# Optimization experiments

Measured on AMD Instinct MI355X. Metric: run time of the kernel, lower is better.

The kernel has to match this reference:

```python
import jax, jax.numpy as jnp
import numpy as np

NUM_EMBED = 1024
HEAD_SIZE = 64
B, T = 4, 4096

def setup_inputs() -> dict:
    key = jax.random.key(0)
    kx, kq, kk, kv = jax.random.split(key, 4)
    scale = NUM_EMBED ** -0.5
    return {
        "x": jax.random.normal(kx, (B, T, NUM_EMBED), dtype=jnp.float32),
        "Wq": jax.random.normal(kq, (NUM_EMBED, HEAD_SIZE), dtype=jnp.float32) * scale,
        "Wk": jax.random.normal(kk, (NUM_EMBED, HEAD_SIZE), dtype=jnp.float32) * scale,
        "Wv": jax.random.normal(kv, (NUM_EMBED, HEAD_SIZE), dtype=jnp.float32) * scale,
    }

def reference(x, Wq, Wk, Wv):
    # x: [B,T,C]; Wq/Wk/Wv: [C,H]
    q = jnp.einsum('btc,ch->bth', x, Wq)
    k = jnp.einsum('btc,ch->bth', x, Wk)
    v = jnp.einsum('btc,ch->bth', x, Wv)
    Tq = x.shape[1]
    att = jnp.einsum('bth,bsh->bts', q, k) * (k.shape[-1] ** -0.5)  # [B,T,T]
    causal = jnp.tril(jnp.ones((Tq, Tq), dtype=bool))
    att = jnp.where(causal, att, -jnp.inf)
    att = jax.nn.softmax(att, axis=-1)
    # dropout p=0 (eval mode): identity
    out = jnp.einsum('bts,bsh->bth', att, v)  # [B,T,H]
    return out
```

## Files before the change

### kernel.cpp

```cpp
#include <hip/hip_runtime.h>

#define B_ 4
#define T_ 4096
#define C_ 1024
#define H_ 64

typedef _Float16 half8  __attribute__((ext_vector_type(8)));
typedef _Float16 half4_ __attribute__((ext_vector_type(4)));
typedef float    floatx4 __attribute__((ext_vector_type(4)));

#define MFMA16(a, b, c) __builtin_amdgcn_mfma_f32_16x16x32_f16(a, b, c, 0, 0, 0)

__global__ __launch_bounds__(256) void pack_w_kn(
    const float* __restrict__ Wq, const float* __restrict__ Wk,
    const float* __restrict__ Wv, _Float16* __restrict__ Wt2)
{
    const int idx  = blockIdx.x * 256 + threadIdx.x;
    const int mt   = idx >> 14;
    const int j    = (idx >> 10) & 15;
    const int f    = (idx >> 9) & 1;
    const int lane = (idx >> 3) & 63;
    const int jj   = idx & 7;
    const int q = lane >> 4, c = lane & 15;
    const int k  = j * 64 + f * 32 + q * 8 + jj;
    const int hp = mt * 16 + c;
    const float* W = (hp < 64) ? Wq : (hp < 128) ? Wk : Wv;
    Wt2[idx] = (_Float16)W[k * H_ + (hp & 63)];
}

__global__ __launch_bounds__(512) void qkv_kn(
    const float* __restrict__ x, const _Float16* __restrict__ Wt2,
    _Float16* __restrict__ Qh, _Float16* __restrict__ Kpk,
    _Float16* __restrict__ Vpk)
{
    __shared__ _Float16 xs[2][32][72];
    const int tid  = threadIdx.x;
    const int lane = tid & 63, w = tid >> 6;
    const int q    = lane >> 4, c = lane & 15;
    const int nt   = w & 1;
    const int mg   = w >> 1;
    const int row0 = blockIdx.x * 32;

    const int srow = tid >> 4, scol = (tid & 15) * 4;
    const float* xg = x + (size_t)(row0 + srow) * C_ + scol;

    floatx4 acc[3];
    #pragma unroll
    for (int i = 0; i < 3; ++i) acc[i] = floatx4{0.f, 0.f, 0.f, 0.f};

    float4 g = *(const float4*)xg;

    for (int j = 0; j < 16; ++j) {
        half4_ hv;
        hv[0] = (_Float16)g.x; hv[1] = (_Float16)g.y;
        hv[2] = (_Float16)g.z; hv[3] = (_Float16)g.w;
        *(half4_*)(&xs[j & 1][srow][scol]) = hv;
        __syncthreads();
        if (j < 15) g = *(const float4*)(xg + (j + 1) * 64);

        const _Float16* xrow = &xs[j & 1][nt * 16 + c][q * 8];
        const half8 b0 = *(const half8*)xrow;
        const half8 b1 = *(const half8*)(xrow + 32);

        half8 a[6];
        #pragma unroll
        for (int i = 0; i < 3; ++i) {
            const size_t fb = ((size_t)((mg * 3 + i) * 16 + j) * 2) * 512 + lane * 8;
            a[i * 2]     = *(const half8*)(Wt2 + fb);
            a[i * 2 + 1] = *(const half8*)(Wt2 + fb + 512);
        }
        #pragma unroll
        for (int i = 0; i < 3; ++i) {
            acc[i] = MFMA16(a[i * 2],     b0, acc[i]);
            acc[i] = MFMA16(a[i * 2 + 1], b1, acc[i]);
        }
    }

    const int row = row0 + nt * 16 + c;
    const int b = row >> 12, t4 = row & (T_ - 1);
    const int kt = t4 >> 6;
    const size_t tbase = ((size_t)b * 64 + kt) * 4096;
    const int mtk = (t4 >> 4) & 3;
    const int kk  = t4 & 63;

    #pragma unroll
    for (int i = 0; i < 3; ++i) {
        const int gi = mg * 3 + i;
        if (gi < 4) {
            half4_ v;
            #pragma unroll
            for (int r = 0; r < 4; ++r) v[r] = (_Float16)acc[i][r];
            *(half4_*)(Qh + (size_t)row * H_ + gi * 16 + q * 4) = v;
        } else if (gi < 8) {
            half4_ v;
            #pragma unroll
            for (int r = 0; r < 4; ++r) v[r] = (_Float16)acc[i][r];
            const int e  = gi - 4;
            const int f  = e >> 1;
            const int qa = (e * 2 + (q >> 1)) & 3;
            *(half4_*)(Kpk + tbase + ((size_t)(mtk * 2 + f) * 64 + qa * 16 + c) * 8
                       + (q & 1) * 4) = v;
        } else {
            const int mtv = gi - 8;
            const int qa = (kk >> 3) & 3, fv = kk >> 5, jv = kk & 7;
            #pragma unroll
            for (int r = 0; r < 4; ++r) {
                const int cv = q * 4 + r;
                Vpk[tbase + ((size_t)(mtv * 2 + fv) * 64 + qa * 16 + cv) * 8 + jv]
                    = (_Float16)acc[i][r];
            }
        }
    }
}

__global__ __launch_bounds__(512, 4) void attn_kn(
    const _Float16* __restrict__ Qh, const _Float16* __restrict__ Kpk,
    const _Float16* __restrict__ Vpk, float* __restrict__ out)
{
    __shared__ __align__(16) char smem[36864];
    const int lane = threadIdx.x & 63;
    const int w    = threadIdx.x >> 6;
    const int q    = lane >> 4, c = lane & 15;
    const int b    = blockIdx.y;
    const int t    = 255 - (int)blockIdx.x;
    const int row0 = t * 16;
    const int grow = b * T_ + row0;
    const int nk   = (t >> 2) + 1;

    _Float16* Pw = (_Float16*)smem + w * 2304;

    half8 bq0 = *(const half8*)(Qh + (size_t)(grow + c) * H_ + q * 8);
    half8 bq1 = *(const half8*)(Qh + (size_t)(grow + c) * H_ + 32 + q * 8);
    const _Float16 qs = (_Float16)0.18033688f;
    bq0 *= qs; bq1 *= qs;

    floatx4 o[4];
    #pragma unroll
    for (int i = 0; i < 4; ++i) o[i] = floatx4{0.f, 0.f, 0.f, 0.f};
    float m = -3.0e38f, l = 0.f;

    for (int kt = w; kt < nk; kt += 8) {
        const int kb = kt * 64;
        const _Float16* Kt = Kpk + ((size_t)b * 64 + kt) * 4096;
        const _Float16* Vt = Vpk + ((size_t)b * 64 + kt) * 4096;
        half8 a0[4], a1[4];

        #pragma unroll
        for (int mt = 0; mt < 4; ++mt) {
            a0[mt] = *(const half8*)(Kt + ((size_t)(mt * 2)     * 64 + lane) * 8);
            a1[mt] = *(const half8*)(Kt + ((size_t)(mt * 2 + 1) * 64 + lane) * 8);
        }
        floatx4 s[4];
        #pragma unroll
        for (int mt = 0; mt < 4; ++mt) {
            floatx4 z = floatx4{0.f, 0.f, 0.f, 0.f};
            z = MFMA16(a0[mt], bq0, z);
            s[mt] = MFMA16(a1[mt], bq1, z);
        }
        #pragma unroll
        for (int mt = 0; mt < 4; ++mt) {
            a0[mt] = *(const half8*)(Vt + ((size_t)(mt * 2)     * 64 + lane) * 8);
            a1[mt] = *(const half8*)(Vt + ((size_t)(mt * 2 + 1) * 64 + lane) * 8);
        }

        if (kt == nk - 1) {
            #pragma unroll
            for (int mt = 0; mt < 4; ++mt)
                #pragma unroll
                for (int r = 0; r < 4; ++r)
                    if (kb + mt * 16 + q * 4 + r > row0 + c) s[mt][r] = -3.0e38f;
        }

        float mx = s[0][0];
        #pragma unroll
        for (int mt = 0; mt < 4; ++mt)
            #pragma unroll
            for (int r = 0; r < 4; ++r) mx = fmaxf(mx, s[mt][r]);
        mx = fmaxf(mx, __shfl_xor(mx, 16, 64));
        mx = fmaxf(mx, __shfl_xor(mx, 32, 64));
        const float mn    = fmaxf(m, mx);
        const float alpha = exp2f(m - mn);
        float p[4][4];
        float sl = 0.f;
        #pragma unroll
        for (int mt = 0; mt < 4; ++mt)
            #pragma unroll
            for (int r = 0; r < 4; ++r) {
                p[mt][r] = exp2f(s[mt][r] - mn);
                sl += p[mt][r];
            }
        sl += __shfl_xor(sl, 16, 64);
        sl += __shfl_xor(sl, 32, 64);
        l = l * alpha + sl;
        m = mn;
        #pragma unroll
        for (int mt = 0; mt < 4; ++mt)
            #pragma unroll
            for (int r = 0; r < 4; ++r) o[mt][r] *= alpha;

        _Float16* pl = Pw + ((kt >> 3) & 1) * 1152 + c * 72;
        #pragma unroll
        for (int mt = 0; mt < 4; ++mt) {
            half4_ ph;
            #pragma unroll
            for (int r = 0; r < 4; ++r) ph[r] = (_Float16)p[mt][r];
            *(half4_*)(pl + mt * 16 + q * 4) = ph;
        }
        const half8 bp0 = *(const half8*)(pl + q * 8);
        const half8 bp1 = *(const half8*)(pl + 32 + q * 8);

        #pragma unroll
        for (int mt = 0; mt < 4; ++mt) {
            o[mt] = MFMA16(a0[mt], bp0, o[mt]);
            o[mt] = MFMA16(a1[mt], bp1, o[mt]);
        }
    }

    __syncthreads();
    float* Ol = (float*)smem;
    float* Ml = (float*)(smem + 34816);
    float* Ll = (float*)(smem + 35328);
    if (q == 0) Ml[w * 16 + c] = m;
    __syncthreads();
    float M = Ml[c];
    #pragma unroll
    for (int w2 = 1; w2 < 8; ++w2) M = fmaxf(M, Ml[w2 * 16 + c]);
    const float alpha = exp2f(m - M);
    if (q == 0) Ll[w * 16 + c] = l * alpha;
    #pragma unroll
    for (int mt = 0; mt < 4; ++mt)
        #pragma unroll
        for (int r = 0; r < 4; ++r)
            Ol[w * 1088 + (mt * 16 + q * 4 + r) * 17 + c] = o[mt][r] * alpha;
    __syncthreads();

    float L = 0.f;
    #pragma unroll
    for (int w2 = 0; w2 < 8; ++w2) L += Ll[w2 * 16 + c];
    const float inv = 1.f / L;
    const int h0 = w * 8 + q * 2;
    float ox = 0.f, oy = 0.f;
    #pragma unroll
    for (int w2 = 0; w2 < 8; ++w2) {
        ox += Ol[w2 * 1088 + h0 * 17 + c];
        oy += Ol[w2 * 1088 + (h0 + 1) * 17 + c];
    }
    float2 st; st.x = ox * inv; st.y = oy * inv;
    *(float2*)(out + (size_t)(grow + c) * H_ + h0) = st;
}

extern "C" void kernel_launch(void* const* d_in, const int* in_sizes, int n_in,
                              void* d_out, int out_size, void* d_ws, size_t ws_size,
                              hipStream_t stream) {
    const float* x  = (const float*)d_in[0];
    const float* Wq = (const float*)d_in[1];
    const float* Wk = (const float*)d_in[2];
    const float* Wv = (const float*)d_in[3];
    float* out = (float*)d_out;

    _Float16* ws = (_Float16*)d_ws;
    _Float16* Wt2 = ws;
    _Float16* Qh  = ws + 196608;
    _Float16* Kpk = Qh + 1048576;
    _Float16* Vpk = Kpk + 1048576;

    hipLaunchKernelGGL(pack_w_kn, dim3(768), dim3(256), 0, stream, Wq, Wk, Wv, Wt2);
    hipLaunchKernelGGL(qkv_kn, dim3((B_ * T_) / 32), dim3(512), 0, stream,
                       x, Wt2, Qh, Kpk, Vpk);
    hipLaunchKernelGGL(attn_kn, dim3(T_ / 16, B_), dim3(512), 0, stream,
                       Qh, Kpk, Vpk, out);
}
```

Before: 142.7 us.

## Process two query/row tiles per wave to reuse K/V and weight fragments

The attention kernel now handles 32 query rows per block, two 16-row tiles per wave. Each K/V fragment loaded from global memory feeds twice as many MFMAs, which halves K/V traffic and the number of blocks. The QKV projection kernel likewise uses 4 waves that each cover both 16-row halves, so each weight fragment is reused twice. The cost is more registers: attention launch bounds drop to 3 blocks per SM, and the finishing reduction runs twice with extra barriers.

```diff
diff --git a/kernel.cpp b/kernel.cpp
--- a/kernel.cpp
+++ b/kernel.cpp
@@ -28,7 +28,7 @@
     Wt2[idx] = (_Float16)W[k * H_ + (hp & 63)];
 }
 
-__global__ __launch_bounds__(512) void qkv_kn(
+__global__ __launch_bounds__(256, 4) void qkv_kn(
     const float* __restrict__ x, const _Float16* __restrict__ Wt2,
     _Float16* __restrict__ Qh, _Float16* __restrict__ Kpk,
     _Float16* __restrict__ Vpk)
@@ -37,83 +37,93 @@
     const int tid  = threadIdx.x;
     const int lane = tid & 63, w = tid >> 6;
     const int q    = lane >> 4, c = lane & 15;
-    const int nt   = w & 1;
-    const int mg   = w >> 1;
     const int row0 = blockIdx.x * 32;
 
-    const int srow = tid >> 4, scol = (tid & 15) * 4;
-    const float* xg = x + (size_t)(row0 + srow) * C_ + scol;
-
-    floatx4 acc[3];
+    const int r1 = tid >> 4, c1 = (tid & 15) * 4;
+    const float* xg1 = x + (size_t)(row0 + r1) * C_ + c1;
+    const float* xg2 = xg1 + 16 * C_;
+
+    floatx4 acc[3][2];
     #pragma unroll
-    for (int i = 0; i < 3; ++i) acc[i] = floatx4{0.f, 0.f, 0.f, 0.f};
-
-    float4 g = *(const float4*)xg;
+    for (int i = 0; i < 3; ++i)
+        #pragma unroll
+        for (int n = 0; n < 2; ++n) acc[i][n] = floatx4{0.f, 0.f, 0.f, 0.f};
+
+    float4 g1 = *(const float4*)xg1;
+    float4 g2 = *(const float4*)xg2;
 
     for (int j = 0; j < 16; ++j) {
-        half4_ hv;
-        hv[0] = (_Float16)g.x; hv[1] = (_Float16)g.y;
-        hv[2] = (_Float16)g.z; hv[3] = (_Float16)g.w;
-        *(half4_*)(&xs[j & 1][srow][scol]) = hv;
+        half4_ h1, h2;
+        h1[0] = (_Float16)g1.x; h1[1] = (_Float16)g1.y;
+        h1[2] = (_Float16)g1.z; h1[3] = (_Float16)g1.w;
+        h2[0] = (_Float16)g2.x; h2[1] = (_Float16)g2.y;
+        h2[2] = (_Float16)g2.z; h2[3] = (_Float16)g2.w;
+        *(half4_*)(&xs[j & 1][r1][c1])      = h1;
+        *(half4_*)(&xs[j & 1][r1 + 16][c1]) = h2;
         __syncthreads();
-        if (j < 15) g = *(const float4*)(xg + (j + 1) * 64);
-
-        const _Float16* xrow = &xs[j & 1][nt * 16 + c][q * 8];
-        const half8 b0 = *(const half8*)xrow;
-        const half8 b1 = *(const half8*)(xrow + 32);
-
-        half8 a[6];
+        if (j < 15) {
+            g1 = *(const float4*)(xg1 + (j + 1) * 64);
+            g2 = *(const float4*)(xg2 + (j + 1) * 64);
+        }
+
+        const half8 b0 = *(const half8*)(&xs[j & 1][c][q * 8]);
+        const half8 b1 = *(const half8*)(&xs[j & 1][c][32 + q * 8]);
+        const half8 b2 = *(const half8*)(&xs[j & 1][16 + c][q * 8]);
+        const half8 b3 = *(const half8*)(&xs[j & 1][16 + c][32 + q * 8]);
+
         #pragma unroll
         for (int i = 0; i < 3; ++i) {
-            const size_t fb = ((size_t)((mg * 3 + i) * 16 + j) * 2) * 512 + lane * 8;
-            a[i * 2]     = *(const half8*)(Wt2 + fb);
-            a[i * 2 + 1] = *(const half8*)(Wt2 + fb + 512);
-        }
+            const size_t fb = ((size_t)((w * 3 + i) * 16 + j) * 2) * 512 + lane * 8;
+            const half8 a0 = *(const half8*)(Wt2 + fb);
+            const half8 a1 = *(const half8*)(Wt2 + fb + 512);
+            acc[i][0] = MFMA16(a0, b0, acc[i][0]);
+            acc[i][0] = MFMA16(a1, b1, acc[i][0]);
+            acc[i][1] = MFMA16(a0, b2, acc[i][1]);
+            acc[i][1] = MFMA16(a1, b3, acc[i][1]);
+        }
+    }
+
+    #pragma unroll
+    for (int n = 0; n < 2; ++n) {
+        const int row = row0 + n * 16 + c;
+        const int b = row >> 12, t4 = row & (T_ - 1);
+        const int kt = t4 >> 6;
+        const size_t tbase = ((size_t)b * 64 + kt) * 4096;
+        const int mtk = (t4 >> 4) & 3;
+        const int kk  = t4 & 63;
         #pragma unroll
         for (int i = 0; i < 3; ++i) {
-            acc[i] = MFMA16(a[i * 2],     b0, acc[i]);
-            acc[i] = MFMA16(a[i * 2 + 1], b1, acc[i]);
-        }
-    }
-
-    const int row = row0 + nt * 16 + c;
-    const int b = row >> 12, t4 = row & (T_ - 1);
-    const int kt = t4 >> 6;
-    const size_t tbase = ((size_t)b * 64 + kt) * 4096;
-    const int mtk = (t4 >> 4) & 3;
-    const int kk  = t4 & 63;
-
-    #pragma unroll
-    for (int i = 0; i < 3; ++i) {
-        const int gi = mg * 3 + i;
-        if (gi < 4) {
-            half4_ v;
-            #pragma unroll
-            for (int r = 0; r < 4; ++r) v[r] = (_Float16)acc[i][r];
-            *(half4_*)(Qh + (size_t)row * H_ + gi * 16 + q * 4) = v;
-        } else if (gi < 8) {
-            half4_ v;
-            #pragma unroll
-            for (int r = 0; r < 4; ++r) v[r] = (_Float16)acc[i][r];
-            const int e  = gi - 4;
-            const int f  = e >> 1;
-            const int qa = (e * 2 + (q >> 1)) & 3;
-            *(half4_*)(Kpk + tbase + ((size_t)(mtk * 2 + f) * 64 + qa * 16 + c) * 8
-                       + (q & 1) * 4) = v;
-        } else {
-            const int mtv = gi - 8;
-            const int qa = (kk >> 3) & 3, fv = kk >> 5, jv = kk & 7;
-            #pragma unroll
-            for (int r = 0; r < 4; ++r) {
-                const int cv = q * 4 + r;
-                Vpk[tbase + ((size_t)(mtv * 2 + fv) * 64 + qa * 16 + cv) * 8 + jv]
-                    = (_Float16)acc[i][r];
+            const int gi = w * 3 + i;
+            if (gi < 4) {
+                half4_ v;
+                #pragma unroll
+                for (int r = 0; r < 4; ++r) v[r] = (_Float16)acc[i][n][r];
+                *(half4_*)(Qh + (size_t)row * H_ + gi * 16 + q * 4) = v;
+            } else if (gi < 8) {
+                half4_ v;
+                #pragma unroll
+                for (int r = 0; r < 4; ++r) v[r] = (_Float16)acc[i][n][r];
+                const int e  = gi - 4;
+                const int f  = e >> 1;
+                const int qa = (e * 2 + (q >> 1)) & 3;
+                *(half4_*)(Kpk + tbase
+                           + ((size_t)(mtk * 2 + f) * 64 + qa * 16 + c) * 8
+                           + (q & 1) * 4) = v;
+            } else {
+                const int mtv = gi - 8;
+                const int qa = (kk >> 3) & 3, fv = kk >> 5, jv = kk & 7;
+                #pragma unroll
+                for (int r = 0; r < 4; ++r) {
+                    const int cv = q * 4 + r;
+                    Vpk[tbase + ((size_t)(mtv * 2 + fv) * 64 + qa * 16 + cv) * 8
+                        + jv] = (_Float16)acc[i][n][r];
+                }
             }
         }
     }
 }
 
-__global__ __launch_bounds__(512, 4) void attn_kn(
+__global__ __launch_bounds__(512, 3) void attn_kn(
     const _Float16* __restrict__ Qh, const _Float16* __restrict__ Kpk,
     const _Float16* __restrict__ Vpk, float* __restrict__ out)
 {
@@ -122,131 +132,184 @@
     const int w    = threadIdx.x >> 6;
     const int q    = lane >> 4, c = lane & 15;
     const int b    = blockIdx.y;
-    const int t    = 255 - (int)blockIdx.x;
-    const int row0 = t * 16;
+    const int t32  = 127 - (int)blockIdx.x;
+    const int row0 = t32 * 32;
     const int grow = b * T_ + row0;
-    const int nk   = (t >> 2) + 1;
-
-    _Float16* Pw = (_Float16*)smem + w * 2304;
-
+    const int nk   = (t32 >> 1) + 1;
+
+    _Float16* pl0 = (_Float16*)smem + w * 2304 + c * 72;
+    _Float16* pl1 = pl0 + 1152;
+
+    const _Float16 qs = (_Float16)0.18033688f;
     half8 bq0 = *(const half8*)(Qh + (size_t)(grow + c) * H_ + q * 8);
     half8 bq1 = *(const half8*)(Qh + (size_t)(grow + c) * H_ + 32 + q * 8);
-    const _Float16 qs = (_Float16)0.18033688f;
-    bq0 *= qs; bq1 *= qs;
-
-    floatx4 o[4];
+    half8 bq2 = *(const half8*)(Qh + (size_t)(grow + 16 + c) * H_ + q * 8);
+    half8 bq3 = *(const half8*)(Qh + (size_t)(grow + 16 + c) * H_ + 32 + q * 8);
+    bq0 *= qs; bq1 *= qs; bq2 *= qs; bq3 *= qs;
+
+    floatx4 o0[4], o1[4];
     #pragma unroll
-    for (int i = 0; i < 4; ++i) o[i] = floatx4{0.f, 0.f, 0.f, 0.f};
-    float m = -3.0e38f, l = 0.f;
+    for (int i = 0; i < 4; ++i) {
+        o0[i] = floatx4{0.f, 0.f, 0.f, 0.f};
+        o1[i] = floatx4{0.f, 0.f, 0.f, 0.f};
+    }
+    float m0 = -3.0e38f, l0 = 0.f, m1 = -3.0e38f, l1 = 0.f;
 
     for (int kt = w; kt < nk; kt += 8) {
         const int kb = kt * 64;
         const _Float16* Kt = Kpk + ((size_t)b * 64 + kt) * 4096;
         const _Float16* Vt = Vpk + ((size_t)b * 64 + kt) * 4096;
-        half8 a0[4], a1[4];
-
-        #pragma unroll
-        for (int mt = 0; mt < 4; ++mt) {
-            a0[mt] = *(const half8*)(Kt + ((size_t)(mt * 2)     * 64 + lane) * 8);
-            a1[mt] = *(const half8*)(Kt + ((size_t)(mt * 2 + 1) * 64 + lane) * 8);
-        }
-        floatx4 s[4];
+
+        half8 ka[4], kb8[4];
+        #pragma unroll
+        for (int mt = 0; mt < 4; ++mt) {
+            ka[mt]  = *(const half8*)(Kt + ((size_t)(mt * 2)     * 64 + lane) * 8);
+            kb8[mt] = *(const half8*)(Kt + ((size_t)(mt * 2 + 1) * 64 + lane) * 8);
+        }
+        floatx4 s0[4], s1[4];
         #pragma unroll
         for (int mt = 0; mt < 4; ++mt) {
             floatx4 z = floatx4{0.f, 0.f, 0.f, 0.f};
-            z = MFMA16(a0[mt], bq0, z);
-            s[mt] = MFMA16(a1[mt], bq1, z);
-        }
-        #pragma unroll
-        for (int mt = 0; mt < 4; ++mt) {
-            a0[mt] = *(const half8*)(Vt + ((size_t)(mt * 2)     * 64 + lane) * 8);
-            a1[mt] = *(const half8*)(Vt + ((size_t)(mt * 2 + 1) * 64 + lane) * 8);
+            z = MFMA16(ka[mt], bq0, z);
+            s0[mt] = MFMA16(kb8[mt], bq1, z);
+        }
+        half8 va[4], vb[4];
+        #pragma unroll
+        for (int mt = 0; mt < 4; ++mt) {
+            va[mt] = *(const half8*)(Vt + ((size_t)(mt * 2)     * 64 + lane) * 8);
+            vb[mt] = *(const half8*)(Vt + ((size_t)(mt * 2 + 1) * 64 + lane) * 8);
+        }
+        #pragma unroll
+        for (int mt = 0; mt < 4; ++mt) {
+            floatx4 z = floatx4{0.f, 0.f, 0.f, 0.f};
+            z = MFMA16(ka[mt], bq2, z);
+            s1[mt] = MFMA16(kb8[mt], bq3, z);
         }
 
         if (kt == nk - 1) {
             #pragma unroll
             for (int mt = 0; mt < 4; ++mt)
                 #pragma unroll
-                for (int r = 0; r < 4; ++r)
-                    if (kb + mt * 16 + q * 4 + r > row0 + c) s[mt][r] = -3.0e38f;
-        }
-
-        float mx = s[0][0];
-        #pragma unroll
-        for (int mt = 0; mt < 4; ++mt)
-            #pragma unroll
-            for (int r = 0; r < 4; ++r) mx = fmaxf(mx, s[mt][r]);
-        mx = fmaxf(mx, __shfl_xor(mx, 16, 64));
-        mx = fmaxf(mx, __shfl_xor(mx, 32, 64));
-        const float mn    = fmaxf(m, mx);
-        const float alpha = exp2f(m - mn);
-        float p[4][4];
-        float sl = 0.f;
-        #pragma unroll
-        for (int mt = 0; mt < 4; ++mt)
-            #pragma unroll
-            for (int r = 0; r < 4; ++r) {
-                p[mt][r] = exp2f(s[mt][r] - mn);
-                sl += p[mt][r];
+                for (int r = 0; r < 4; ++r) {
+                    const int key = kb + mt * 16 + q * 4 + r;
+                    if (key > row0 + c)      s0[mt][r] = -3.0e38f;
+                    if (key > row0 + 16 + c) s1[mt][r] = -3.0e38f;
+                }
+        }
+
+        {
+            float mx = s0[0][0];
+            #pragma unroll
+            for (int mt = 0; mt < 4; ++mt)
+                #pragma unroll
+                for (int r = 0; r < 4; ++r) mx = fmaxf(mx, s0[mt][r]);
+            mx = fmaxf(mx, __shfl_xor(mx, 16, 64));
+            mx = fmaxf(mx, __shfl_xor(mx, 32, 64));
+            const float mn    = fmaxf(m0, mx);
+            const float alpha = exp2f(m0 - mn);
+            float sl = 0.f;
+            #pragma unroll
+            for (int mt = 0; mt < 4; ++mt) {
+                half4_ ph;
+                #pragma unroll
+                for (int r = 0; r < 4; ++r) {
+                    const float p = exp2f(s0[mt][r] - mn);
+                    sl += p;
+                    ph[r] = (_Float16)p;
+                }
+                *(half4_*)(pl0 + mt * 16 + q * 4) = ph;
             }
-        sl += __shfl_xor(sl, 16, 64);
-        sl += __shfl_xor(sl, 32, 64);
-        l = l * alpha + sl;
-        m = mn;
-        #pragma unroll
-        for (int mt = 0; mt < 4; ++mt)
-            #pragma unroll
-            for (int r = 0; r < 4; ++r) o[mt][r] *= alpha;
-
-        _Float16* pl = Pw + ((kt >> 3) & 1) * 1152 + c * 72;
-        #pragma unroll
-        for (int mt = 0; mt < 4; ++mt) {
-            half4_ ph;
-            #pragma unroll
-            for (int r = 0; r < 4; ++r) ph[r] = (_Float16)p[mt][r];
-            *(half4_*)(pl + mt * 16 + q * 4) = ph;
-        }
-        const half8 bp0 = *(const half8*)(pl + q * 8);
-        const half8 bp1 = *(const half8*)(pl + 32 + q * 8);
-
-        #pragma unroll
-        for (int mt = 0; mt < 4; ++mt) {
-            o[mt] = MFMA16(a0[mt], bp0, o[mt]);
-            o[mt] = MFMA16(a1[mt], bp1, o[mt]);
-        }
-    }
-
-    __syncthreads();
+            sl += __shfl_xor(sl, 16, 64);
+            sl += __shfl_xor(sl, 32, 64);
+            l0 = l0 * alpha + sl;
+            m0 = mn;
+            #pragma unroll
+            for (int mt = 0; mt < 4; ++mt)
+                #pragma unroll
+                for (int r = 0; r < 4; ++r) o0[mt][r] *= alpha;
+        }
+        {
+            float mx = s1[0][0];
+            #pragma unroll
+            for (int mt = 0; mt < 4; ++mt)
+                #pragma unroll
+                for (int r = 0; r < 4; ++r) mx = fmaxf(mx, s1[mt][r]);
+            mx = fmaxf(mx, __shfl_xor(mx, 16, 64));
+            mx = fmaxf(mx, __shfl_xor(mx, 32, 64));
+            const float mn    = fmaxf(m1, mx);
+            const float alpha = exp2f(m1 - mn);
+            float sl = 0.f;
+            #pragma unroll
+            for (int mt = 0; mt < 4; ++mt) {
+                half4_ ph;
+                #pragma unroll
+                for (int r = 0; r < 4; ++r) {
+                    const float p = exp2f(s1[mt][r] - mn);
+                    sl += p;
+                    ph[r] = (_Float16)p;
+                }
+                *(half4_*)(pl1 + mt * 16 + q * 4) = ph;
+            }
+            sl += __shfl_xor(sl, 16, 64);
+            sl += __shfl_xor(sl, 32, 64);
+            l1 = l1 * alpha + sl;
+            m1 = mn;
+            #pragma unroll
+            for (int mt = 0; mt < 4; ++mt)
+                #pragma unroll
+                for (int r = 0; r < 4; ++r) o1[mt][r] *= alpha;
+        }
+
+        const half8 bp0 = *(const half8*)(pl0 + q * 8);
+        const half8 bp1 = *(const half8*)(pl0 + 32 + q * 8);
+        const half8 bp2 = *(const half8*)(pl1 + q * 8);
+        const half8 bp3 = *(const half8*)(pl1 + 32 + q * 8);
+
+        #pragma unroll
+        for (int mt = 0; mt < 4; ++mt) {
+            o0[mt] = MFMA16(va[mt], bp0, o0[mt]);
+            o0[mt] = MFMA16(vb[mt], bp1, o0[mt]);
+            o1[mt] = MFMA16(va[mt], bp2, o1[mt]);
+            o1[mt] = MFMA16(vb[mt], bp3, o1[mt]);
+        }
+    }
+
     float* Ol = (float*)smem;
     float* Ml = (float*)(smem + 34816);
     float* Ll = (float*)(smem + 35328);
-    if (q == 0) Ml[w * 16 + c] = m;
-    __syncthreads();
-    float M = Ml[c];
     #pragma unroll
-    for (int w2 = 1; w2 < 8; ++w2) M = fmaxf(M, Ml[w2 * 16 + c]);
-    const float alpha = exp2f(m - M);
-    if (q == 0) Ll[w * 16 + c] = l * alpha;
-    #pragma unroll
-    for (int mt = 0; mt < 4; ++mt)
-        #pragma unroll
-        for (int r = 0; r < 4; ++r)
-            Ol[w * 1088 + (mt * 16 + q * 4 + r) * 17 + c] = o[mt][r] * alpha;
-    __syncthreads();
-
-    float L = 0.f;
-    #pragma unroll
-    for (int w2 = 0; w2 < 8; ++w2) L += Ll[w2 * 16 + c];
-    const float inv = 1.f / L;
-    const int h0 = w * 8 + q * 2;
-    float ox = 0.f, oy = 0.f;
-    #pragma unroll
-    for (int w2 = 0; w2 < 8; ++w2) {
-        ox += Ol[w2 * 1088 + h0 * 17 + c];
-        oy += Ol[w2 * 1088 + (h0 + 1) * 17 + c];
-    }
-    float2 st; st.x = ox * inv; st.y = oy * inv;
-    *(float2*)(out + (size_t)(grow + c) * H_ + h0) = st;
+    for (int ph = 0; ph < 2; ++ph) {
+        const float     mm = ph ? m1 : m0;
+        const float     ll = ph ? l1 : l0;
+        const floatx4* oo  = ph ? o1 : o0;
+        __syncthreads();
+        if (q == 0) Ml[w * 16 + c] = mm;
+        __syncthreads();
+        float M = Ml[c];
+        #pragma unroll
+        for (int w2 = 1; w2 < 8; ++w2) M = fmaxf(M, Ml[w2 * 16 + c]);
+        const float alpha = exp2f(mm - M);
+        if (q == 0) Ll[w * 16 + c] = ll * alpha;
+        #pragma unroll
+        for (int mt = 0; mt < 4; ++mt)
+            #pragma unroll
+            for (int r = 0; r < 4; ++r)
+                Ol[w * 1088 + (mt * 16 + q * 4 + r) * 17 + c] = oo[mt][r] * alpha;
+        __syncthreads();
+        float L = 0.f;
+        #pragma unroll
+        for (int w2 = 0; w2 < 8; ++w2) L += Ll[w2 * 16 + c];
+        const float inv = 1.f / L;
+        const int h0 = w * 8 + q * 2;
+        float ox = 0.f, oy = 0.f;
+        #pragma unroll
+        for (int w2 = 0; w2 < 8; ++w2) {
+            ox += Ol[w2 * 1088 + h0 * 17 + c];
+            oy += Ol[w2 * 1088 + (h0 + 1) * 17 + c];
+        }
+        float2 st; st.x = ox * inv; st.y = oy * inv;
+        *(float2*)(out + (size_t)(grow + ph * 16 + c) * H_ + h0) = st;
+    }
 }
 
 extern "C" void kernel_launch(void* const* d_in, const int* in_sizes, int n_in,
@@ -265,8 +328,8 @@
     _Float16* Vpk = Kpk + 1048576;
 
     hipLaunchKernelGGL(pack_w_kn, dim3(768), dim3(256), 0, stream, Wq, Wk, Wv, Wt2);
-    hipLaunchKernelGGL(qkv_kn, dim3((B_ * T_) / 32), dim3(512), 0, stream,
+    hipLaunchKernelGGL(qkv_kn, dim3((B_ * T_) / 32), dim3(256), 0, stream,
                        x, Wt2, Qh, Kpk, Vpk);
-    hipLaunchKernelGGL(attn_kn, dim3(T_ / 16, B_), dim3(512), 0, stream,
+    hipLaunchKernelGGL(attn_kn, dim3(T_ / 32, B_), dim3(512), 0, stream,
                        Qh, Kpk, Vpk, out);
 }
```

Result: slower. 152.4 us (+6.8%).
